# Performance work log

Measured on AMD Instinct MI355X. Metric: run time of the kernel, lower is better.

## Reference

```python
import jax, jax.numpy as jnp
import numpy as np

LOW_T, HIGH_T = 100.0, 200.0  # cv2.Canny thresholds from source


def _conv3(x, k):
    # x: [B,H,W], k: [3,3]; replicate border like OpenCV BORDER_REPLICATE
    xp = jnp.pad(x, ((0, 0), (1, 1), (1, 1)), mode='edge')
    return jax.lax.conv_general_dilated(
        xp[:, None], k[None, None].astype(x.dtype),
        window_strides=(1, 1), padding='VALID')[:, 0]


def _shift(a, dy, dx):
    # zero-padded spatial shift: result[y,x] = a[y+dy, x+dx]
    B, H, W = a.shape
    ap = jnp.pad(a, ((0, 0), (1, 1), (1, 1)))
    return ap[:, 1 + dy:1 + dy + H, 1 + dx:1 + dx + W]


def canny(labels):
    # (labels*255).astype(uint8) quantization, kept as float
    img = jnp.floor(jnp.clip(labels, 0.0, 1.0) * 255.0)
    kx = jnp.array([[-1., 0., 1.], [-2., 0., 2.], [-1., 0., 1.]], img.dtype)
    ky = jnp.array([[-1., -2., -1.], [0., 0., 0.], [1., 2., 1.]], img.dtype)
    gx = _conv3(img, kx)
    gy = _conv3(img, ky)
    mag = jnp.abs(gx) + jnp.abs(gy)  # OpenCV default L1 gradient
    theta = jnp.mod(jnp.degrees(jnp.arctan2(gy, gx)), 180.0)
    b0 = (theta < 22.5) | (theta >= 157.5)
    b45 = (theta >= 22.5) & (theta < 67.5)
    b90 = (theta >= 67.5) & (theta < 112.5)
    # neighbors along gradient direction (non-maximum suppression)
    n1 = jnp.where(b0, _shift(mag, 0, 1),
         jnp.where(b45, _shift(mag, -1, 1),
         jnp.where(b90, _shift(mag, 1, 0), _shift(mag, -1, -1))))
    n2 = jnp.where(b0, _shift(mag, 0, -1),
         jnp.where(b45, _shift(mag, 1, -1),
         jnp.where(b90, _shift(mag, -1, 0), _shift(mag, 1, 1))))
    nms = (mag >= n1) & (mag >= n2)
    strong = nms & (mag > HIGH_T)
    weak = nms & (mag > LOW_T)

    def dilate(e):
        return jax.lax.reduce_window(e.astype(jnp.float32), 0.0, jax.lax.max,
                                     (1, 3, 3), (1, 1, 1), 'SAME') > 0

    # hysteresis: grow strong edges through weak pixels to fixpoint
    def body(state):
        e, _ = state
        ne = weak & dilate(e)
        return ne, jnp.any(ne != e)

    edges, _ = jax.lax.while_loop(lambda s: s[1], body, (strong, jnp.array(True)))
    return edges.astype(jnp.int32)  # binary {0,1} edge mask


def setup_inputs() -> dict:
    key = jax.random.key(0)
    k1, k2 = jax.random.split(key)
    pred = jax.random.normal(k1, (32, 2, 512, 512), dtype=jnp.float32)
    labels = jax.random.uniform(k2, (32, 512, 512), dtype=jnp.float32)
    return {"pred": pred, "labels": labels}


def reference(pred, labels):
    edge_mask = canny(labels)  # [B,H,W] int in {0,1}
    logp = jax.nn.log_softmax(pred, axis=1)  # [B,2,H,W]
    nll = -jnp.take_along_axis(logp, edge_mask[:, None], axis=1)[:, 0]
    return nll.mean()
```

## Files before the change

### kernel.cpp

```cpp
#include <hip/hip_runtime.h>
#include <hip/hip_fp16.h>

typedef unsigned long long u64;
typedef unsigned int u32;
typedef unsigned char u8;

#define IMH 512
#define IMW 512
#define NB 32
#define WPI 4096
#define NWORDS (NB*WPI)

#define QZ(v) floorf(fminf(fmaxf((v),0.f),1.f)*255.f)

#define LOADRAW(Y, V, HL, HR) do { \
    int _yc = (Y); _yc = _yc < 0 ? 0 : (_yc > 511 ? 511 : _yc); \
    const float* _row = img + _yc*IMW; \
    V = *(const float4*)&_row[xb]; \
    if (L0)  HL = *(const float2*)&_row[strip ? (X0-2) : 0]; \
    if (L63) HR = *(const float2*)&_row[strip ? 510 : (X0+256)]; \
} while(0)

#define NMSJ(J, QAm, QA0, QAp, PBm, PB0, PBp, CCm, CC0, CCp) do { \
    float m = PB0; \
    float gx_ = gxP[J], gy_ = gyP[J]; \
    float ax = fabsf(gx_), ay = fabsf(gy_); \
    bool c0_ = ay <  T1f*ax; \
    bool c90 = ay >= T2f*ax; \
    bool c45 = (!c0_) && (!c90) && (gx_*gy_ > 0.f); \
    float n1 = c0_ ? PBp : (c45 ? QAp : (c90 ? CC0 : QAm)); \
    float n2 = c0_ ? PBm : (c45 ? CCm : (c90 ? QA0 : CCp)); \
    if (m >= n1 && m >= n2) { \
        if (m > 100.f) wb |= (1u<<(J)); \
        if (m > 200.f) sb |= (1u<<(J)); \
    } \
} while(0)

#define STEP(Y, VIN, HLIN, HRIN, VNX, HLNX, HRNX, DOLOAD) do { \
    if (DOLOAD) LOADRAW((Y)+1, VNX, HLNX, HRNX); \
    float c0=QZ(VIN.x), c1=QZ(VIN.y), c2=QZ(VIN.z), c3=QZ(VIN.w); \
    float chl0 = QZ(HLIN.x), chl1 = strip ? QZ(HLIN.y) : QZ(HLIN.x); \
    float chr0 = strip ? QZ(HRIN.y) : QZ(HRIN.x), chr1 = QZ(HRIN.y); \
    float qn0=rP[0]+c0, qn1=rP[1]+c1, qn2=rP[2]+c2, qn3=rP[3]+c3; \
    float ql0=hPl0+chl0, ql1=hPl1+chl1, qr0=hPr0+chr0, qr1=hPr1+chr1; \
    float t1_0=qP[0]+qn0, t1_1=qP[1]+qn1, t1_2=qP[2]+qn2, t1_3=qP[3]+qn3; \
    float t2_0=qn0-qP[0], t2_1=qn1-qP[1], t2_2=qn2-qP[2], t2_3=qn3-qP[3]; \
    float t1l0=qPl0+ql0, t2l0=ql0-qPl0, t1l1=qPl1+ql1, t2l1=ql1-qPl1; \
    float t1r0=qPr0+qr0, t2r0=qr0-qPr0, t1r1=qPr1+qr1, t2r1=qr1-qPr1; \
    float su1=__shfl_up(t1_3,1), su2=__shfl_up(t2_3,1); \
    float sd1=__shfl_down(t1_0,1), sd2=__shfl_down(t2_0,1); \
    float t1m = L0 ? t1l1 : su1, t2m = L0 ? t2l1 : su2; \
    float t1p = L63 ? t1r0 : sd1, t2p = L63 ? t2r0 : sd2; \
    const int ry = (Y)-1; \
    const bool rok = (ry >= 0) && (ry <= 511); \
    float gxc0 = t1_1-t1m,  gyc0 = t2m +2.f*t2_0+t2_1; \
    float gxc1 = t1_2-t1_0, gyc1 = t2_0+2.f*t2_1+t2_2; \
    float gxc2 = t1_3-t1_1, gyc2 = t2_1+2.f*t2_2+t2_3; \
    float gxc3 = t1p -t1_2, gyc3 = t2_2+2.f*t2_3+t2p; \
    float mc0 = rok ? fabsf(gxc0)+fabsf(gyc0) : 0.f; \
    float mc1 = rok ? fabsf(gxc1)+fabsf(gyc1) : 0.f; \
    float mc2 = rok ? fabsf(gxc2)+fabsf(gyc2) : 0.f; \
    float mc3 = rok ? fabsf(gxc3)+fabsf(gyc3) : 0.f; \
    float gxl = t1_0-t1l0, gyl = t2l0+2.f*t2l1+t2_0; \
    float gxr = t1r1-t1_3, gyr = t2_3+2.f*t2r0+t2r1; \
    float mlh = (rok && strip!=0) ? fabsf(gxl)+fabsf(gyl) : 0.f; \
    float mrh = (rok && strip!=1) ? fabsf(gxr)+fabsf(gyr) : 0.f; \
    float sum_ = __shfl_up(mc3,1), sdm_ = __shfl_down(mc0,1); \
    float mCL = L0 ? mlh : sum_; \
    float mCR = L63 ? mrh : sdm_; \
    if ((Y) >= y0+2) { \
        u32 sb=0, wb=0; \
        NMSJ(0, mgQL,  mgQ[0], mgQ[1], mgPL,  mgP[0], mgP[1], mCL, mc0, mc1); \
        NMSJ(1, mgQ[0],mgQ[1], mgQ[2], mgP[0],mgP[1], mgP[2], mc0, mc1, mc2); \
        NMSJ(2, mgQ[1],mgQ[2], mgQ[3], mgP[1],mgP[2], mgP[3], mc1, mc2, mc3); \
        NMSJ(3, mgQ[2],mgQ[3], mgQR,   mgP[2],mgP[3], mgPR,   mc2, mc3, mCR); \
        u32 pk = sb | (wb<<8); \
        u32 oth = __shfl_xor(pk, 1); \
        if (!(lane & 1)) { \
            size_t bix = ((size_t)(bimg*IMH + ((Y)-2)))*64 + strip*32 + (lane>>1); \
            edgeb[bix] = (u8)((sb & 0xFu) | ((oth & 0xFu) << 4)); \
            weakb[bix] = (u8)(((pk>>8) & 0xFu) | (((oth>>8) & 0xFu) << 4)); \
        } \
    } \
    mgQ[0]=mgP[0]; mgQ[1]=mgP[1]; mgQ[2]=mgP[2]; mgQ[3]=mgP[3]; \
    mgQL=mgPL; mgQR=mgPR; \
    mgP[0]=mc0; mgP[1]=mc1; mgP[2]=mc2; mgP[3]=mc3; \
    mgPL=mCL; mgPR=mCR; \
    gxP[0]=gxc0; gxP[1]=gxc1; gxP[2]=gxc2; gxP[3]=gxc3; \
    gyP[0]=gyc0; gyP[1]=gyc1; gyP[2]=gyc2; gyP[3]=gyc3; \
    qP[0]=qn0; qP[1]=qn1; qP[2]=qn2; qP[3]=qn3; \
    qPl0=ql0; qPl1=ql1; qPr0=qr0; qPr1=qr1; \
    rP[0]=c0; rP[1]=c1; rP[2]=c2; rP[3]=c3; \
    hPl0=chl0; hPl1=chl1; hPr0=chr0; hPr1=chr1; \
} while(0)

__device__ __forceinline__ void sobel_wave(
    const float* __restrict__ labels,
    u8* __restrict__ edgeb,
    u8* __restrict__ weakb,
    int vbx, int lane)
{
    const int bimg  = vbx >> 7;
    const int strip = vbx & 1;
    const int band  = (vbx >> 1) & 63;
    const int X0 = strip*256;
    const int y0 = band*8;
    const int xb = X0 + 4*lane;
    const bool L0 = (lane==0), L63 = (lane==63);
    const float* img = labels + (size_t)bimg*(IMH*IMW);
    const float T1f = 0.41421356237309503f;
    const float T2f = 2.4142135623730951f;

    float rP[4];
    float hPl0,hPl1,hPr0,hPr1;
    float qP[4];
    float qPl0,qPl1,qPr0,qPr1;
    float mgQ[4], mgP[4];
    float mgQL,mgQR,mgPL,mgPR;
    float gxP[4], gyP[4];

    float4 vA, vB;
    float2 hlA = make_float2(0.f,0.f), hlB = make_float2(0.f,0.f);
    float2 hrA = make_float2(0.f,0.f), hrB = make_float2(0.f,0.f);

    LOADRAW(y0-2, vA, hlA, hrA);
    LOADRAW(y0-1, vB, hlB, hrB);
    {
        float a0=QZ(vA.x), a1=QZ(vA.y), a2=QZ(vA.z), a3=QZ(vA.w);
        float b0=QZ(vB.x), b1=QZ(vB.y), b2=QZ(vB.z), b3=QZ(vB.w);
        qP[0]=a0+b0; qP[1]=a1+b1; qP[2]=a2+b2; qP[3]=a3+b3;
        rP[0]=b0; rP[1]=b1; rP[2]=b2; rP[3]=b3;
        float al0 = QZ(hlA.x), al1 = strip ? QZ(hlA.y) : QZ(hlA.x);
        float ar0 = strip ? QZ(hrA.y) : QZ(hrA.x), ar1 = QZ(hrA.y);
        hPl0 = QZ(hlB.x); hPl1 = strip ? QZ(hlB.y) : QZ(hlB.x);
        hPr0 = strip ? QZ(hrB.y) : QZ(hrB.x); hPr1 = QZ(hrB.y);
        qPl0 = al0 + hPl0; qPl1 = al1 + hPl1;
        qPr0 = ar0 + hPr0; qPr1 = ar1 + hPr1;
    }
#pragma unroll
    for (int j=0;j<4;++j) { mgQ[j]=0.f; mgP[j]=0.f; gxP[j]=0.f; gyP[j]=0.f; }
    mgQL=mgQR=mgPL=mgPR=0.f;

    LOADRAW(y0, vA, hlA, hrA);

#pragma unroll 1
    for (int y = y0; y < y0+10; y += 2) {
        STEP(y,   vA, hlA, hrA, vB, hlB, hrB, (y+1 <= y0+9));
        STEP(y+1, vB, hlB, hrB, vA, hlA, hrA, (y+2 <= y0+9));
    }
}

__global__ __launch_bounds__(256) void k_front(
    const float* __restrict__ pred,
    const float* __restrict__ labels,
    u8* __restrict__ edgeb,
    u8* __restrict__ weakb,
    u32* __restrict__ dpack,
    double* __restrict__ partial,
    int store_d)
{
    if (blockIdx.x < 2048) {
        const int t = blockIdx.x*256 + threadIdx.x;
        float4 P0[4], P1[4];
#pragma unroll
        for (int k = 0; k < 4; ++k) {
            int g = t + k*524288;
            int b = g >> 16, rem4 = g & 65535;
            P0[k] = *(const float4*)&pred[((size_t)(2*b)  <<18) + 4*(size_t)rem4];
            P1[k] = *(const float4*)&pred[((size_t)(2*b+1)<<18) + 4*(size_t)rem4];
        }
        __builtin_amdgcn_sched_barrier(0);
        float acc[4];
        uint2 st[4];
#pragma unroll
        for (int k = 0; k < 4; ++k) {
            float d0=P1[k].x-P0[k].x, d1=P1[k].y-P0[k].y;
            float d2=P1[k].z-P0[k].z, d3=P1[k].w-P0[k].w;
            float s0 = fmaxf(d0,0.f) + __logf(1.f + __expf(-fabsf(d0)));
            float s1 = fmaxf(d1,0.f) + __logf(1.f + __expf(-fabsf(d1)));
            float s2 = fmaxf(d2,0.f) + __logf(1.f + __expf(-fabsf(d2)));
            float s3 = fmaxf(d3,0.f) + __logf(1.f + __expf(-fabsf(d3)));
            acc[k] = (s0+s1)+(s2+s3);
            __half2 h01 = __floats2half2_rn(d0,d1);
            __half2 h23 = __floats2half2_rn(d2,d3);
            st[k].x = *(u32*)&h01;
            st[k].y = *(u32*)&h23;
        }
        if (store_d) {
#pragma unroll
            for (int k = 0; k < 4; ++k) {
                int g = t + k*524288;
                ((uint2*)dpack)[g] = st[k];
            }
        }
        double s = ((double)acc[0]+(double)acc[1]) + ((double)acc[2]+(double)acc[3]);
#pragma unroll
        for (int off = 32; off > 0; off >>= 1) s += __shfl_down(s, off);
        __shared__ double sh[4];
        if ((threadIdx.x & 63) == 0) sh[threadIdx.x>>6] = s;
        __syncthreads();
        if (threadIdx.x == 0) partial[blockIdx.x] = (sh[0]+sh[1])+(sh[2]+sh[3]);
    } else {
        sobel_wave(labels, edgeb, weakb,
                   (blockIdx.x - 2048)*4 + (threadIdx.x >> 6),
                   threadIdx.x & 63);
    }
}

#define H2ROWS 64
#define H2HALO 32
#define H2LDSR 128

__device__ inline u64 hz3(u64 l, u64 c, u64 r) {
    return c | (c<<1) | (c>>1) | (l>>63) | (r<<63);
}

template<int MODE>
__global__ __launch_bounds__(256) void k_hyst(
    const u64* __restrict__ edgew,
    const u64* __restrict__ weakw,
    const u32* __restrict__ dpack,
    const float* __restrict__ pred,
    double* __restrict__ partial)
{
    __shared__ u64 ed[H2LDSR][9];
    __shared__ u64 wk[H2LDSR][9];
    __shared__ int s_chg;
    const int tid = threadIdx.x;
    const int strip = blockIdx.x & 7, b = blockIdx.x >> 3;
    const int y0 = strip*H2ROWS;
    const u64* eb = edgew + (size_t)b*WPI;
    const u64* wb = weakw + (size_t)b*WPI;

#pragma unroll
    for (int k = 0; k < 4; ++k) {
        int w = tid + k*256;
        int r = w >> 3, c = w & 7;
        int gr = y0 - H2HALO + r;
        u64 e = 0, ww = 0;
        if (gr >= 0 && gr < IMH) { e = eb[gr*8+c]; ww = wb[gr*8+c]; }
        ed[r][c] = e; wk[r][c] = ww;
    }
    const int c  = tid & 7;
    const int r0 = 4*(tid >> 3);
    __syncthreads();

    for (int iter = 0; iter < 32; ++iter) {
        if (tid == 0) s_chg = 0;
        __syncthreads();
        u64 H[6];
#pragma unroll
        for (int j = 0; j < 6; ++j) {
            int r = r0 - 1 + j;
            u64 lm = 0, cc = 0, rr = 0;
            if (r >= 0 && r < H2LDSR) {
                cc = ed[r][c];
                lm = (c > 0) ? ed[r][c-1] : 0;
                rr = (c < 7) ? ed[r][c+1] : 0;
            }
            H[j] = hz3(lm, cc, rr);
        }
        bool chg = false;
#pragma unroll
        for (int i = 0; i < 4; ++i) {
            u64 old = ed[r0+i][c];
            u64 nw  = wk[r0+i][c] & (H[i] | H[i+1] | H[i+2]);
            if (nw != old) { ed[r0+i][c] = nw; chg = true; }
        }
        if (chg) s_chg = 1;
        __syncthreads();
        if (s_chg == 0) break;
    }

    const int c8 = tid >> 5;
    const u32 s2 = (u32)((2*tid) & 63);
    double es = 0.0;
    if (MODE) {
        const u32* dp = dpack + (((size_t)b*IMH + y0) << 8);
#pragma unroll 8
        for (int r = 0; r < 64; ++r) {
            u32 pk = dp[(r<<8) + tid];
            u64 w = ed[H2HALO + r][c8];
            float2 f = __half22float2(*(__half2*)&pk);
            if ((w >> s2) & 1)     es += (double)f.x;
            if ((w >> (s2+1)) & 1) es += (double)f.y;
        }
    } else {
        const float* pb0 = pred + (((size_t)(2*b))<<18) + (size_t)y0*IMW;
        const float* pb1 = pb0 + (1<<18);
#pragma unroll 4
        for (int r = 0; r < 64; ++r) {
            float2 a0 = *(const float2*)&pb0[r*IMW + 2*tid];
            float2 a1 = *(const float2*)&pb1[r*IMW + 2*tid];
            u64 w = ed[H2HALO + r][c8];
            if ((w >> s2) & 1)     es += (double)(a1.x - a0.x);
            if ((w >> (s2+1)) & 1) es += (double)(a1.y - a0.y);
        }
    }
#pragma unroll
    for (int off = 32; off > 0; off >>= 1) es += __shfl_down(es, off);
    __shared__ double shq[4];
    if ((tid & 63) == 0) shq[tid>>6] = es;
    __syncthreads();
    if (tid == 0) partial[2048 + blockIdx.x] = (shq[0]+shq[1])+(shq[2]+shq[3]);
}

__global__ __launch_bounds__(256) void k_final2(
    const double* __restrict__ partial, float* __restrict__ out)
{
    double s = 0.0;
    for (int i = threadIdx.x; i < 2048; i += 256) s += partial[i];
    double v = s - partial[2048 + threadIdx.x];
#pragma unroll
    for (int off = 32; off > 0; off >>= 1) v += __shfl_down(v, off);
    __shared__ double sh[4];
    if ((threadIdx.x & 63) == 0) sh[threadIdx.x>>6] = v;
    __syncthreads();
    if (threadIdx.x == 0)
        out[0] = (float)(((sh[0]+sh[1])+(sh[2]+sh[3])) * (1.0/8388608.0));
}

extern "C" void kernel_launch(void* const* d_in, const int* in_sizes, int n_in,
                              void* d_out, int out_size, void* d_ws, size_t ws_size,
                              hipStream_t stream)
{
    const float* pred   = (const float*)d_in[0];
    const float* labels = (const float*)d_in[1];
    float* out = (float*)d_out;

    char* ws = (char*)d_ws;
    double* partial = (double*)ws;
    u64*    edgew   = (u64*)(ws + 32768);
    u64*    weakw   = edgew + NWORDS;
    u32*    dpack   = (u32*)(ws + 32768 + 2*(size_t)NWORDS*8);
    const size_t need = 32768 + 2*(size_t)NWORDS*8 + (size_t)4194304*4;
    const int use_dpack = (ws_size >= need) ? 1 : 0;

    k_front<<<3072, 256, 0, stream>>>(pred, labels, (u8*)edgew, (u8*)weakw,
                                      dpack, partial, use_dpack);
    if (use_dpack)
        k_hyst<1><<<256, 256, 0, stream>>>(edgew, weakw, dpack, pred, partial);
    else
        k_hyst<0><<<256, 256, 0, stream>>>(edgew, weakw, dpack, pred, partial);
    k_final2<<<1, 256, 0, stream>>>(partial, out);
}
```

Before: 47.16 us.

## Drop fp16 difference buffer and interleave sobel and softplus blocks

Removes the packed half-precision pred-difference buffer that the front kernel wrote and the hysteresis kernel read back. The hysteresis kernel now re-reads both fp32 pred channels directly. The front kernel's grid is also reordered so every third block runs the Sobel/NMS work, interleaved with the softplus-reduction blocks, so both kinds of work share the machine concurrently instead of running as two back-to-back groups. This trades a 16MB write plus 16MB read for a 32MB re-read of pred, which may partly hit in cache.

Result: slower. 64.08 us (+35.9%).

```diff
diff --git a/kernel.cpp b/kernel.cpp
--- a/kernel.cpp
+++ b/kernel.cpp
@@ -1,5 +1,4 @@
 #include <hip/hip_runtime.h>
-#include <hip/hip_fp16.h>
 
 typedef unsigned long long u64;
 typedef unsigned int u32;
@@ -150,61 +149,49 @@
     }
 }
 
-__global__ __launch_bounds__(256) void k_front(
+__global__ __launch_bounds__(256) void k_front2(
     const float* __restrict__ pred,
     const float* __restrict__ labels,
     u8* __restrict__ edgeb,
     u8* __restrict__ weakb,
-    u32* __restrict__ dpack,
-    double* __restrict__ partial,
-    int store_d)
-{
-    if (blockIdx.x < 2048) {
-        const int t = blockIdx.x*256 + threadIdx.x;
-        float4 P0[4], P1[4];
-#pragma unroll
-        for (int k = 0; k < 4; ++k) {
-            int g = t + k*524288;
-            int b = g >> 16, rem4 = g & 65535;
-            P0[k] = *(const float4*)&pred[((size_t)(2*b)  <<18) + 4*(size_t)rem4];
-            P1[k] = *(const float4*)&pred[((size_t)(2*b+1)<<18) + 4*(size_t)rem4];
-        }
-        __builtin_amdgcn_sched_barrier(0);
-        float acc[4];
-        uint2 st[4];
-#pragma unroll
-        for (int k = 0; k < 4; ++k) {
-            float d0=P1[k].x-P0[k].x, d1=P1[k].y-P0[k].y;
-            float d2=P1[k].z-P0[k].z, d3=P1[k].w-P0[k].w;
-            float s0 = fmaxf(d0,0.f) + __logf(1.f + __expf(-fabsf(d0)));
-            float s1 = fmaxf(d1,0.f) + __logf(1.f + __expf(-fabsf(d1)));
-            float s2 = fmaxf(d2,0.f) + __logf(1.f + __expf(-fabsf(d2)));
-            float s3 = fmaxf(d3,0.f) + __logf(1.f + __expf(-fabsf(d3)));
-            acc[k] = (s0+s1)+(s2+s3);
-            __half2 h01 = __floats2half2_rn(d0,d1);
-            __half2 h23 = __floats2half2_rn(d2,d3);
-            st[k].x = *(u32*)&h01;
-            st[k].y = *(u32*)&h23;
-        }
-        if (store_d) {
-#pragma unroll
-            for (int k = 0; k < 4; ++k) {
-                int g = t + k*524288;
-                ((uint2*)dpack)[g] = st[k];
-            }
-        }
-        double s = ((double)acc[0]+(double)acc[1]) + ((double)acc[2]+(double)acc[3]);
-#pragma unroll
-        for (int off = 32; off > 0; off >>= 1) s += __shfl_down(s, off);
-        __shared__ double sh[4];
-        if ((threadIdx.x & 63) == 0) sh[threadIdx.x>>6] = s;
-        __syncthreads();
-        if (threadIdx.x == 0) partial[blockIdx.x] = (sh[0]+sh[1])+(sh[2]+sh[3]);
-    } else {
+    double* __restrict__ partial)
+{
+    const int bx = blockIdx.x;
+    const int m3 = bx % 3;
+    if (m3 == 2) {
         sobel_wave(labels, edgeb, weakb,
-                   (blockIdx.x - 2048)*4 + (threadIdx.x >> 6),
-                   threadIdx.x & 63);
-    }
+                   (bx/3)*4 + (threadIdx.x >> 6), threadIdx.x & 63);
+        return;
+    }
+    const int lid = (bx/3)*2 + m3;
+    const int t = lid*256 + threadIdx.x;
+    float4 P0[4], P1[4];
+#pragma unroll
+    for (int k = 0; k < 4; ++k) {
+        int g = t + k*524288;
+        int b = g >> 16, rem4 = g & 65535;
+        P0[k] = *(const float4*)&pred[((size_t)(2*b)  <<18) + 4*(size_t)rem4];
+        P1[k] = *(const float4*)&pred[((size_t)(2*b+1)<<18) + 4*(size_t)rem4];
+    }
+    __builtin_amdgcn_sched_barrier(0);
+    float acc[4];
+#pragma unroll
+    for (int k = 0; k < 4; ++k) {
+        float d0=P1[k].x-P0[k].x, d1=P1[k].y-P0[k].y;
+        float d2=P1[k].z-P0[k].z, d3=P1[k].w-P0[k].w;
+        float s0 = fmaxf(d0,0.f) + __logf(1.f + __expf(-fabsf(d0)));
+        float s1 = fmaxf(d1,0.f) + __logf(1.f + __expf(-fabsf(d1)));
+        float s2 = fmaxf(d2,0.f) + __logf(1.f + __expf(-fabsf(d2)));
+        float s3 = fmaxf(d3,0.f) + __logf(1.f + __expf(-fabsf(d3)));
+        acc[k] = (s0+s1)+(s2+s3);
+    }
+    double s = ((double)acc[0]+(double)acc[1]) + ((double)acc[2]+(double)acc[3]);
+#pragma unroll
+    for (int off = 32; off > 0; off >>= 1) s += __shfl_down(s, off);
+    __shared__ double sh[4];
+    if ((threadIdx.x & 63) == 0) sh[threadIdx.x>>6] = s;
+    __syncthreads();
+    if (threadIdx.x == 0) partial[lid] = (sh[0]+sh[1])+(sh[2]+sh[3]);
 }
 
 #define H2ROWS 64
@@ -215,11 +202,9 @@
     return c | (c<<1) | (c>>1) | (l>>63) | (r<<63);
 }
 
-template<int MODE>
-__global__ __launch_bounds__(256) void k_hyst(
+__global__ __launch_bounds__(256) void k_hyst_sum(
     const u64* __restrict__ edgew,
     const u64* __restrict__ weakw,
-    const u32* __restrict__ dpack,
     const float* __restrict__ pred,
     double* __restrict__ partial)
 {
@@ -275,27 +260,15 @@
     const int c8 = tid >> 5;
     const u32 s2 = (u32)((2*tid) & 63);
     double es = 0.0;
-    if (MODE) {
-        const u32* dp = dpack + (((size_t)b*IMH + y0) << 8);
-#pragma unroll 8
-        for (int r = 0; r < 64; ++r) {
-            u32 pk = dp[(r<<8) + tid];
-            u64 w = ed[H2HALO + r][c8];
-            float2 f = __half22float2(*(__half2*)&pk);
-            if ((w >> s2) & 1)     es += (double)f.x;
-            if ((w >> (s2+1)) & 1) es += (double)f.y;
-        }
-    } else {
-        const float* pb0 = pred + (((size_t)(2*b))<<18) + (size_t)y0*IMW;
-        const float* pb1 = pb0 + (1<<18);
+    const float* pb0 = pred + (((size_t)(2*b))<<18) + (size_t)y0*IMW;
+    const float* pb1 = pb0 + (1<<18);
 #pragma unroll 4
-        for (int r = 0; r < 64; ++r) {
-            float2 a0 = *(const float2*)&pb0[r*IMW + 2*tid];
-            float2 a1 = *(const float2*)&pb1[r*IMW + 2*tid];
-            u64 w = ed[H2HALO + r][c8];
-            if ((w >> s2) & 1)     es += (double)(a1.x - a0.x);
-            if ((w >> (s2+1)) & 1) es += (double)(a1.y - a0.y);
-        }
+    for (int r = 0; r < 64; ++r) {
+        float2 a0 = *(const float2*)&pb0[r*IMW + 2*tid];
+        float2 a1 = *(const float2*)&pb1[r*IMW + 2*tid];
+        u64 w = ed[H2HALO + r][c8];
+        if ((w >> s2) & 1)     es += (double)(a1.x - a0.x);
+        if ((w >> (s2+1)) & 1) es += (double)(a1.y - a0.y);
     }
 #pragma unroll
     for (int off = 32; off > 0; off >>= 1) es += __shfl_down(es, off);
@@ -305,7 +278,7 @@
     if (tid == 0) partial[2048 + blockIdx.x] = (shq[0]+shq[1])+(shq[2]+shq[3]);
 }
 
-__global__ __launch_bounds__(256) void k_final2(
+__global__ __launch_bounds__(256) void k_final3(
     const double* __restrict__ partial, float* __restrict__ out)
 {
     double s = 0.0;
@@ -332,15 +305,8 @@
     double* partial = (double*)ws;
     u64*    edgew   = (u64*)(ws + 32768);
     u64*    weakw   = edgew + NWORDS;
-    u32*    dpack   = (u32*)(ws + 32768 + 2*(size_t)NWORDS*8);
-    const size_t need = 32768 + 2*(size_t)NWORDS*8 + (size_t)4194304*4;
-    const int use_dpack = (ws_size >= need) ? 1 : 0;
-
-    k_front<<<3072, 256, 0, stream>>>(pred, labels, (u8*)edgew, (u8*)weakw,
-                                      dpack, partial, use_dpack);
-    if (use_dpack)
-        k_hyst<1><<<256, 256, 0, stream>>>(edgew, weakw, dpack, pred, partial);
-    else
-        k_hyst<0><<<256, 256, 0, stream>>>(edgew, weakw, dpack, pred, partial);
-    k_final2<<<1, 256, 0, stream>>>(partial, out);
-}
+
+    k_front2<<<3072, 256, 0, stream>>>(pred, labels, (u8*)edgew, (u8*)weakw, partial);
+    k_hyst_sum<<<256, 256, 0, stream>>>(edgew, weakw, pred, partial);
+    k_final3<<<1, 256, 0, stream>>>(partial, out);
+}
```
